# Kernel tuning notes

Measured on AMD Instinct MI355X. Metric: run time of the kernel, lower is better.

The kernel has to match this reference:

```python
import jax, jax.numpy as jnp
import numpy as np

N_NODES = 100000
N_EDGES = 6400000
N_ORDERS = 4
EPO = N_EDGES // N_ORDERS  # edges per order
K = 10


def setup_inputs() -> dict:
    key = jax.random.key(0)
    ks = jax.random.split(key, 7)
    x = jax.random.normal(ks[0], (N_NODES, K), dtype=jnp.float32)
    w_mp = jax.random.normal(ks[1], (K, 2 * K), dtype=jnp.float32) * (1.0 / np.sqrt(2 * K))
    b_mp = jax.random.normal(ks[2], (K,), dtype=jnp.float32) * 0.01
    w_out = jax.random.normal(ks[3], (K, K), dtype=jnp.float32) * (1.0 / np.sqrt(K))
    b_out = jax.random.normal(ks[4], (K,), dtype=jnp.float32) * 0.01
    edge_index = jax.random.randint(ks[5], (2, N_EDGES), 0, N_NODES, dtype=jnp.int64)
    orders = jax.random.randint(ks[6], (N_ORDERS, EPO), 0, N_EDGES, dtype=jnp.int64)
    return {"x": x, "w_mp": w_mp, "b_mp": b_mp, "w_out": w_out,
            "b_out": b_out, "edge_index": edge_index, "orders": orders}


def reference(x, w_mp, b_mp, w_out, b_out, edge_index, orders):
    n = x.shape[0]

    def step(h, order_idx):
        ei = edge_index[:, order_idx]            # [2, EPO] edges of this order
        # torch code swaps rows [1,0] before propagate, so in PyG terms:
        # source j = original row 1, target i = original row 0
        dst = ei[0]
        src = ei[1]
        x_i = h[dst]                             # [EPO, K]
        x_j = h[src]                             # [EPO, K]
        msg_in = jnp.concatenate([x_i, x_j - x_i], axis=1)   # [EPO, 2K]
        msg = msg_in @ w_mp.T + b_mp             # [EPO, K]
        aggr = jax.ops.segment_sum(msg, dst, num_segments=n)  # scatter-add
        return aggr + h, None                    # update(): aggr_out + x

    h, _ = jax.lax.scan(step, x, orders)
    return h @ w_out.T + b_out
```

## Files before the change

### kernel.cpp

```cpp
#include <hip/hip_runtime.h>

#define BLK 256
#define CAPB 4608
#define MAXNBD 512
#define MAXK2 2048
#define OVFN 65536
#define WBITS 13
#define W1CAP 8928
#define MAXNW 1024
#define IPTA 32
#define IPT2 18

__global__ void k_init_h(const float* __restrict__ x, float* __restrict__ h, int n) {
    int total = n * 16;
    int gs = gridDim.x * blockDim.x;
    for (int i = blockIdx.x * blockDim.x + threadIdx.x; i < total; i += gs) {
        int row = i >> 4, col = i & 15;
        h[i] = (col < 10) ? x[row * 10 + col] : 0.0f;
    }
}

__global__ __launch_bounds__(512) void k_win(const int* __restrict__ orders,
                                             int total, int epo, int NW,
                                             int* __restrict__ gcnt1,
                                             unsigned* __restrict__ recs1,
                                             int* __restrict__ ovf1_cnt,
                                             unsigned* __restrict__ ovf1) {
    __shared__ int bcnt[MAXNW];
    __shared__ int gbase[MAXNW];
    int t = threadIdx.x;
    for (int i = t; i < NW; i += 512) bcnt[i] = 0;
    __syncthreads();

    size_t base = (size_t)blockIdx.x * (512 * IPTA);
    int st0 = (int)(base / (size_t)epo);
    size_t b1 = (size_t)(st0 + 1) * (size_t)epo;

    unsigned recr[IPTA]; int rr[IPTA];
    #pragma unroll
    for (int q = 0; q < IPTA; ++q) {
        size_t g = base + (size_t)q * 512 + t;
        recr[q] = 0xFFFFFFFFu; rr[q] = 0;
        if (g < (size_t)total) {
            int idx = orders[g];
            int st = (g >= b1) ? (st0 + 1) : st0;
            recr[q] = ((unsigned)st << 23) | (unsigned)idx;
            rr[q] = atomicAdd(&bcnt[idx >> WBITS], 1);
        }
    }
    __syncthreads();
    for (int k = t; k < NW; k += 512) {
        int c = bcnt[k];
        gbase[k] = c ? atomicAdd(&gcnt1[k], c) : 0;
    }
    __syncthreads();
    #pragma unroll
    for (int q = 0; q < IPTA; ++q) {
        if (recr[q] != 0xFFFFFFFFu) {
            int idx = (int)(recr[q] & 0x7FFFFFu);
            int key = idx >> WBITS;
            int pos = gbase[key] + rr[q];
            if (pos < W1CAP)
                recs1[(size_t)key * W1CAP + pos] = recr[q];
            else {
                int o = atomicAdd(ovf1_cnt, 1);
                if (o < OVFN) ovf1[o] = recr[q];
            }
        }
    }
}

__global__ __launch_bounds__(512) void k_bin2(const int* __restrict__ ei, int ne,
                                              const int* __restrict__ gcnt1,
                                              const unsigned* __restrict__ recs1,
                                              int NW, int NBD,
                                              int* __restrict__ gcnt2,
                                              unsigned* __restrict__ recs2,
                                              int* __restrict__ ovf2_cnt,
                                              int2* __restrict__ ovf2) {
    __shared__ int cnt2[MAXK2];
    __shared__ int gbase[MAXK2];
    int t = threadIdx.x;
    int K2 = 4 * NBD;
    for (int i = t; i < K2; i += 512) cnt2[i] = 0;
    __syncthreads();

    int w = blockIdx.x;
    int c = gcnt1[w]; if (c > W1CAP) c = W1CAP;
    const unsigned* strm = recs1 + (size_t)w * W1CAP;

    unsigned recr[IPT2];
    #pragma unroll
    for (int q = 0; q < IPT2; ++q) {
        int r = q * 512 + t;
        recr[q] = (r < c) ? strm[r] : 0xFFFFFFFFu;
    }
    int dv[IPT2], sv[IPT2];
    #pragma unroll
    for (int q = 0; q < IPT2; ++q) {
        dv[q] = 0; sv[q] = 0;
        if (recr[q] != 0xFFFFFFFFu) {
            int idx = (int)(recr[q] & 0x7FFFFFu);
            dv[q] = ei[idx];
            sv[q] = ei[(size_t)ne + idx];
        }
    }
    int meta[IPT2];
    #pragma unroll
    for (int q = 0; q < IPT2; ++q) {
        meta[q] = -1;
        if (recr[q] != 0xFFFFFFFFu) {
            int st = (int)(recr[q] >> 23);
            int key = st * NBD + (dv[q] >> 8);
            int rk = atomicAdd(&cnt2[key], 1);
            meta[q] = (key << 14) | rk;
        }
    }
    __syncthreads();
    for (int k = t; k < K2; k += 512) {
        int cc = cnt2[k];
        gbase[k] = cc ? atomicAdd(&gcnt2[k], cc) : 0;
    }
    __syncthreads();
    #pragma unroll
    for (int q = 0; q < IPT2; ++q) {
        if (meta[q] >= 0) {
            int key = meta[q] >> 14, rk = meta[q] & 16383;
            int pos = gbase[key] + rk;
            unsigned r2 = ((unsigned)(dv[q] & 255) << 20) | (unsigned)sv[q];
            if (pos < CAPB)
                recs2[(size_t)key * CAPB + pos] = r2;
            else {
                int o = atomicAdd(ovf2_cnt, 1);
                if (o < OVFN) {
                    int st = (int)(recr[q] >> 23);
                    ovf2[o] = make_int2((st << 18) | dv[q], sv[q]);
                }
            }
        }
    }
}

#define IPTG ((CAPB + 511) / 512)
template<bool FINAL>
__global__ __launch_bounds__(512) void k_agg2(const float* __restrict__ h_cur,
                                              float* __restrict__ h_next,
                                              const int* __restrict__ gcnt2_st,
                                              const unsigned* __restrict__ recs2_st,
                                              const float* __restrict__ w_mp,
                                              const float* __restrict__ b_mp,
                                              const float* __restrict__ w_out,
                                              const float* __restrict__ b_out,
                                              float* __restrict__ out, int n) {
    __shared__ unsigned srt[CAPB];
    __shared__ int cnts[256];
    __shared__ int sc[256];
    __shared__ int offs[257];
    __shared__ float part[256 * 10];
    __shared__ float Wa[100], Wb[100], Bm[10];
    __shared__ float Wo[100], Bo[10];
    int t = threadIdx.x;
    if (t < 100) {
        int k = t / 10, j = t - k * 10;
        float w1 = w_mp[k * 20 + j];
        float w2 = w_mp[k * 20 + 10 + j];
        Wa[t] = w1 - w2; Wb[t] = w2;
        if (FINAL) Wo[t] = w_out[t];
    }
    if (t < 10) { Bm[t] = b_mp[t]; if (FINAL) Bo[t] = b_out[t]; }
    if (t < 256) cnts[t] = 0;
    __syncthreads();

    int bkt = blockIdx.x;
    int cnt = gcnt2_st[bkt];
    if (cnt > CAPB) cnt = CAPB;
    const unsigned* strm = recs2_st + (size_t)bkt * CAPB;

    unsigned myrec[IPTG];
    #pragma unroll
    for (int q = 0; q < IPTG; ++q) {
        int r = q * 512 + t;
        myrec[q] = 0xFFFFFFFFu;
        if (r < cnt) {
            unsigned rec = strm[r];
            myrec[q] = rec;
            atomicAdd(&cnts[rec >> 20], 1);
        }
    }
    __syncthreads();

    if (t < 256) sc[t] = cnts[t];
    __syncthreads();
    for (int off = 1; off < 256; off <<= 1) {
        int v = (t < 256 && t >= off) ? sc[t - off] : 0;
        __syncthreads();
        if (t < 256) sc[t] += v;
        __syncthreads();
    }
    if (t < 256) offs[t + 1] = sc[t];
    if (t == 0) offs[0] = 0;
    __syncthreads();
    if (t < 256) cnts[t] = offs[t];
    __syncthreads();

    #pragma unroll
    for (int q = 0; q < IPTG; ++q) {
        if (myrec[q] != 0xFFFFFFFFu) {
            int pos = atomicAdd(&cnts[myrec[q] >> 20], 1);
            srt[pos] = myrec[q];
        }
    }
    __syncthreads();

    int node = t & 255, half = t >> 8;
    int b0 = offs[node], m = offs[node + 1] - b0;
    float S[10] = {0,0,0,0,0,0,0,0,0,0};
    for (int p = b0 + half; p < b0 + m; p += 2) {
        int s = (int)(srt[p] & 0xFFFFFu);
        const float* pj = h_cur + (size_t)s * 16;
        float4 a0 = *(const float4*)(pj);
        float4 a1 = *(const float4*)(pj + 4);
        float2 a2 = *(const float2*)(pj + 8);
        S[0] += a0.x; S[1] += a0.y; S[2] += a0.z; S[3] += a0.w;
        S[4] += a1.x; S[5] += a1.y; S[6] += a1.z; S[7] += a1.w;
        S[8] += a2.x; S[9] += a2.y;
    }
    if (half == 1) {
        #pragma unroll
        for (int j = 0; j < 10; ++j) part[node * 10 + j] = S[j];
    }
    __syncthreads();
    if (half == 0) {
        int i = bkt * 256 + node;
        if (i < n) {
            #pragma unroll
            for (int j = 0; j < 10; ++j) S[j] += part[node * 10 + j];
            const float* pi = h_cur + (size_t)i * 16;
            float4 x0 = *(const float4*)(pi);
            float4 x1 = *(const float4*)(pi + 4);
            float2 x2 = *(const float2*)(pi + 8);
            float xi[10] = {x0.x, x0.y, x0.z, x0.w, x1.x, x1.y, x1.z, x1.w, x2.x, x2.y};
            float deg = (float)m;
            float o[10];
            #pragma unroll
            for (int k = 0; k < 10; ++k) {
                float ma = Bm[k];
                float mb = 0.0f;
                #pragma unroll
                for (int j = 0; j < 10; ++j) {
                    ma += Wa[k * 10 + j] * xi[j];
                    mb += Wb[k * 10 + j] * S[j];
                }
                o[k] = xi[k] + deg * ma + mb;
            }
            if (FINAL) {
                float q2[10];
                #pragma unroll
                for (int k = 0; k < 10; ++k) {
                    float m2 = Bo[k];
                    #pragma unroll
                    for (int j = 0; j < 10; ++j) m2 += Wo[k * 10 + j] * o[j];
                    q2[k] = m2;
                }
                float* po = out + (size_t)i * 10;
                *(float2*)(po)     = make_float2(q2[0], q2[1]);
                *(float2*)(po + 2) = make_float2(q2[2], q2[3]);
                *(float2*)(po + 4) = make_float2(q2[4], q2[5]);
                *(float2*)(po + 6) = make_float2(q2[6], q2[7]);
                *(float2*)(po + 8) = make_float2(q2[8], q2[9]);
            } else {
                float* po = h_next + (size_t)i * 16;
                *(float4*)(po)     = make_float4(o[0], o[1], o[2], o[3]);
                *(float4*)(po + 4) = make_float4(o[4], o[5], o[6], o[7]);
                *(float2*)(po + 8) = make_float2(o[8], o[9]);
            }
        }
    }
}

__global__ void k_fix(const float* __restrict__ h_cur, float* __restrict__ h_next,
                      const int* __restrict__ ei, int ne,
                      const int* __restrict__ ovf1_cnt, const unsigned* __restrict__ ovf1,
                      const int* __restrict__ ovf2_cnt, const int2* __restrict__ ovf2,
                      const float* __restrict__ w_mp, const float* __restrict__ b_mp,
                      int st) {
    __shared__ float Wa[100], Wb[100], Bm[10];
    int t = threadIdx.x;
    if (t < 100) {
        int k = t / 10, j = t - k * 10;
        float w1 = w_mp[k * 20 + j];
        float w2 = w_mp[k * 20 + 10 + j];
        Wa[t] = w1 - w2; Wb[t] = w2;
    }
    if (t < 10) Bm[t] = b_mp[t];
    __syncthreads();
    int c1 = *ovf1_cnt; if (c1 > OVFN) c1 = OVFN;
    int c2 = *ovf2_cnt; if (c2 > OVFN) c2 = OVFN;
    int gs = gridDim.x * blockDim.x;
    for (int i = blockIdx.x * blockDim.x + t; i < c1 + c2; i += gs) {
        int d, s;
        if (i < c1) {
            unsigned v = ovf1[i];
            if ((int)(v >> 23) != st) continue;
            int idx = (int)(v & 0x7FFFFFu);
            d = ei[idx]; s = ei[(size_t)ne + idx];
        } else {
            int2 p = ovf2[i - c1];
            if ((p.x >> 18) != st) continue;
            d = p.x & 0x3FFFF; s = p.y;
        }
        const float* pi = h_cur + (size_t)d * 16;
        const float* pj = h_cur + (size_t)s * 16;
        float xi[10], xj[10];
        #pragma unroll
        for (int j = 0; j < 10; ++j) { xi[j] = pi[j]; xj[j] = pj[j]; }
        float* po = h_next + (size_t)d * 16;
        #pragma unroll
        for (int k = 0; k < 10; ++k) {
            float m = Bm[k];
            #pragma unroll
            for (int j = 0; j < 10; ++j) m += Wa[k * 10 + j] * xi[j] + Wb[k * 10 + j] * xj[j];
            atomicAdd(po + k, m);
        }
    }
}

__global__ void k_fix_final(const float* __restrict__ h_cur, float* __restrict__ out,
                            const int* __restrict__ ei, int ne,
                            const int* __restrict__ ovf1_cnt, const unsigned* __restrict__ ovf1,
                            const int* __restrict__ ovf2_cnt, const int2* __restrict__ ovf2,
                            const float* __restrict__ w_mp, const float* __restrict__ b_mp,
                            const float* __restrict__ w_out, int st) {
    __shared__ float Wa[100], Wb[100], Bm[10], Wo[100];
    int t = threadIdx.x;
    if (t < 100) {
        int k = t / 10, j = t - k * 10;
        float w1 = w_mp[k * 20 + j];
        float w2 = w_mp[k * 20 + 10 + j];
        Wa[t] = w1 - w2; Wb[t] = w2;
        Wo[t] = w_out[t];
    }
    if (t < 10) Bm[t] = b_mp[t];
    __syncthreads();
    int c1 = *ovf1_cnt; if (c1 > OVFN) c1 = OVFN;
    int c2 = *ovf2_cnt; if (c2 > OVFN) c2 = OVFN;
    int gs = gridDim.x * blockDim.x;
    for (int i = blockIdx.x * blockDim.x + t; i < c1 + c2; i += gs) {
        int d, s;
        if (i < c1) {
            unsigned v = ovf1[i];
            if ((int)(v >> 23) != st) continue;
            int idx = (int)(v & 0x7FFFFFu);
            d = ei[idx]; s = ei[(size_t)ne + idx];
        } else {
            int2 p = ovf2[i - c1];
            if ((p.x >> 18) != st) continue;
            d = p.x & 0x3FFFF; s = p.y;
        }
        const float* pi = h_cur + (size_t)d * 16;
        const float* pj = h_cur + (size_t)s * 16;
        float xi[10], xj[10];
        #pragma unroll
        for (int j = 0; j < 10; ++j) { xi[j] = pi[j]; xj[j] = pj[j]; }
        float dm[10];
        #pragma unroll
        for (int k = 0; k < 10; ++k) {
            float m = Bm[k];
            #pragma unroll
            for (int j = 0; j < 10; ++j) m += Wa[k * 10 + j] * xi[j] + Wb[k * 10 + j] * xj[j];
            dm[k] = m;
        }
        float* po = out + (size_t)d * 10;
        #pragma unroll
        for (int q = 0; q < 10; ++q) {
            float m = 0.0f;
            #pragma unroll
            for (int k = 0; k < 10; ++k) m += Wo[q * 10 + k] * dm[k];
            atomicAdd(po + q, m);
        }
    }
}


__global__ void k_init10(const float* __restrict__ x, float* __restrict__ h, int n10) {
    int gs = gridDim.x * blockDim.x;
    for (int i = blockIdx.x * blockDim.x + threadIdx.x; i < n10; i += gs) h[i] = x[i];
}
__global__ void k_copy4(const float4* __restrict__ src, float4* __restrict__ dst, int n4) {
    int gs = gridDim.x * blockDim.x;
    for (int i = blockIdx.x * blockDim.x + threadIdx.x; i < n4; i += gs) dst[i] = src[i];
}
__global__ void k_edge_step10(const float* __restrict__ h_cur, float* __restrict__ h_next,
                              const int* __restrict__ edge_index, const int* __restrict__ order,
                              const float* __restrict__ w_mp, const float* __restrict__ b_mp,
                              int epo, int ne) {
    __shared__ float Wc[200]; __shared__ float Bc[10];
    int t = threadIdx.x;
    if (t < 200) {
        int k = t / 20, j = t - k * 20;
        float w = w_mp[t];
        Wc[t] = (j < 10) ? (w - w_mp[k * 20 + j + 10]) : w;
    }
    if (t < 10) Bc[t] = b_mp[t];
    __syncthreads();
    int gs = gridDim.x * blockDim.x;
    for (int e = blockIdx.x * blockDim.x + t; e < epo; e += gs) {
        int idx = order[e];
        int dst = edge_index[idx];
        int src = edge_index[(size_t)ne + idx];
        const float* pi = h_cur + (size_t)dst * 10;
        const float* pj = h_cur + (size_t)src * 10;
        float xi[10], xj[10];
        #pragma unroll
        for (int j = 0; j < 10; ++j) { xi[j] = pi[j]; xj[j] = pj[j]; }
        float* po = h_next + (size_t)dst * 10;
        #pragma unroll
        for (int k = 0; k < 10; ++k) {
            float m = Bc[k];
            #pragma unroll
            for (int j = 0; j < 10; ++j) m += Wc[k * 20 + j] * xi[j] + Wc[k * 20 + 10 + j] * xj[j];
            atomicAdd(po + k, m);
        }
    }
}
__global__ void k_out10(const float* __restrict__ h, const float* __restrict__ w_out,
                        const float* __restrict__ b_out, float* __restrict__ out, int n) {
    __shared__ float W[100]; __shared__ float B[10];
    int t = threadIdx.x;
    if (t < 100) W[t] = w_out[t];
    if (t < 10)  B[t] = b_out[t];
    __syncthreads();
    int gs = gridDim.x * blockDim.x;
    for (int i = blockIdx.x * blockDim.x + t; i < n; i += gs) {
        float xi[10];
        #pragma unroll
        for (int j = 0; j < 10; ++j) xi[j] = h[(size_t)i * 10 + j];
        #pragma unroll
        for (int k = 0; k < 10; ++k) {
            float m = B[k];
            #pragma unroll
            for (int j = 0; j < 10; ++j) m += W[k * 10 + j] * xi[j];
            out[(size_t)i * 10 + k] = m;
        }
    }
}


extern "C" void kernel_launch(void* const* d_in, const int* in_sizes, int n_in,
                              void* d_out, int out_size, void* d_ws, size_t ws_size,
                              hipStream_t stream) {
    const float* x      = (const float*)d_in[0];
    const float* w_mp   = (const float*)d_in[1];
    const float* b_mp   = (const float*)d_in[2];
    const float* w_out  = (const float*)d_in[3];
    const float* b_out  = (const float*)d_in[4];
    const int*   edge_i = (const int*)d_in[5];
    const int*   orders = (const int*)d_in[6];

    int n  = in_sizes[0] / 10;
    int ne = in_sizes[5] / 2;
    const int n_orders = 4;
    int epo = in_sizes[6] / n_orders;
    int total = n_orders * epo;

    float* out = (float*)d_out;

    int NBD = (n + 255) >> 8;
    int NW  = (ne + (1 << WBITS) - 1) >> WBITS;

    size_t off_hA    = 0;
    size_t off_hB    = off_hA + (size_t)n * 16;
    size_t off_recs1 = off_hB + (size_t)n * 16;
    size_t off_recs2 = off_recs1 + (size_t)NW * W1CAP;
    size_t off_ovf2  = off_recs2 + (size_t)4 * NBD * CAPB;
    size_t off_ovf1  = off_ovf2 + (size_t)2 * OVFN;
    size_t off_gcnt1 = off_ovf1 + OVFN;
    size_t off_gcnt2 = off_gcnt1 + NW;
    size_t off_cnts  = off_gcnt2 + (size_t)4 * NBD;
    size_t need      = (off_cnts + 2) * 4;

    bool ok = (ws_size >= need) && (NW <= MAXNW) && (NBD <= MAXNBD) &&
              (4 * NBD <= MAXK2) && (ne <= (1 << 23)) && (n < (1 << 17));

    if (!ok) {
        float* hA = (float*)d_ws;
        float* hB = hA + (size_t)n * 10;
        int n10 = n * 10;
        hipLaunchKernelGGL(k_init10, dim3(min((n10 + BLK - 1) / BLK, 2048)), dim3(BLK), 0, stream,
                           x, hA, n10);
        int n4 = n10 / 4;
        float* cur = hA; float* nxt = hB;
        int gb_edge = min((epo + BLK - 1) / BLK, 6400);
        for (int s = 0; s < n_orders; ++s) {
            hipLaunchKernelGGL(k_copy4, dim3(min((n4 + BLK - 1) / BLK, 2048)), dim3(BLK), 0, stream,
                               (const float4*)cur, (float4*)nxt, n4);
            hipLaunchKernelGGL(k_edge_step10, dim3(gb_edge), dim3(BLK), 0, stream,
                               cur, nxt, edge_i, orders + (size_t)s * epo, w_mp, b_mp, epo, ne);
            float* t2 = cur; cur = nxt; nxt = t2;
        }
        hipLaunchKernelGGL(k_out10, dim3(min((n + BLK - 1) / BLK, 2048)), dim3(BLK), 0, stream,
                           cur, w_out, b_out, out, n);
        return;
    }

    float*    hA      = (float*)d_ws;
    float*    hB      = (float*)d_ws + off_hB;
    unsigned* recs1   = (unsigned*)d_ws + off_recs1;
    unsigned* recs2   = (unsigned*)d_ws + off_recs2;
    int2*     ovf2    = (int2*)((int*)d_ws + off_ovf2);
    unsigned* ovf1    = (unsigned*)d_ws + off_ovf1;
    int*      gcnt1   = (int*)d_ws + off_gcnt1;
    int*      gcnt2   = (int*)d_ws + off_gcnt2;
    int*      ovfcnts = (int*)d_ws + off_cnts;

    hipMemsetAsync(gcnt1, 0, ((size_t)NW + (size_t)4 * NBD + 2) * sizeof(int), stream);

    int gb_init = min((n * 16 + BLK - 1) / BLK, 2048);
    hipLaunchKernelGGL(k_init_h, dim3(gb_init), dim3(BLK), 0, stream, x, hA, n);

    int gbA = (total + 512 * IPTA - 1) / (512 * IPTA);
    hipLaunchKernelGGL(k_win, dim3(gbA), dim3(512), 0, stream,
                       orders, total, epo, NW, gcnt1, recs1, ovfcnts + 0, ovf1);

    hipLaunchKernelGGL(k_bin2, dim3(NW), dim3(512), 0, stream,
                       edge_i, ne, gcnt1, recs1, NW, NBD,
                       gcnt2, recs2, ovfcnts + 1, ovf2);

    float* cur = hA; float* nxt = hB;
    for (int s = 0; s < n_orders; ++s) {
        bool fin = (s == n_orders - 1);
        if (fin) {
            hipLaunchKernelGGL((k_agg2<true>), dim3(NBD), dim3(512), 0, stream,
                               cur, nxt, gcnt2 + (size_t)s * NBD,
                               recs2 + (size_t)s * NBD * CAPB, w_mp, b_mp,
                               w_out, b_out, out, n);
            hipLaunchKernelGGL(k_fix_final, dim3(8), dim3(256), 0, stream,
                               cur, out, edge_i, ne,
                               ovfcnts + 0, ovf1, ovfcnts + 1, ovf2,
                               w_mp, b_mp, w_out, s);
        } else {
            hipLaunchKernelGGL((k_agg2<false>), dim3(NBD), dim3(512), 0, stream,
                               cur, nxt, gcnt2 + (size_t)s * NBD,
                               recs2 + (size_t)s * NBD * CAPB, w_mp, b_mp,
                               w_out, b_out, out, n);
            hipLaunchKernelGGL(k_fix, dim3(8), dim3(256), 0, stream,
                               cur, nxt, edge_i, ne,
                               ovfcnts + 0, ovf1, ovfcnts + 1, ovf2,
                               w_mp, b_mp, s);
            float* t2 = cur; cur = nxt; nxt = t2;
        }
    }
}
```

Baseline: 286.7 us.

## Partition edge binning per order to shrink shared counters and defer source loads

```diff
diff --git a/kernel.cpp b/kernel.cpp
--- a/kernel.cpp
+++ b/kernel.cpp
@@ -1,15 +1,14 @@
 #include <hip/hip_runtime.h>
 
 #define BLK 256
+#define WBITS 13
+#define W1CAPS 2432
 #define CAPB 4608
+#define MAXNW 1024
 #define MAXNBD 512
-#define MAXK2 2048
 #define OVFN 65536
-#define WBITS 13
-#define W1CAP 8928
-#define MAXNW 1024
-#define IPTA 32
-#define IPT2 18
+#define IPTA 16
+#define NSL 20
 
 __global__ void k_init_h(const float* __restrict__ x, float* __restrict__ h, int n) {
     int total = n * 16;
@@ -21,7 +20,7 @@
 }
 
 __global__ __launch_bounds__(512) void k_win(const int* __restrict__ orders,
-                                             int total, int epo, int NW,
+                                             int epo, int NW, int TPS,
                                              int* __restrict__ gcnt1,
                                              unsigned* __restrict__ recs1,
                                              int* __restrict__ ovf1_cnt,
@@ -29,42 +28,39 @@
     __shared__ int bcnt[MAXNW];
     __shared__ int gbase[MAXNW];
     int t = threadIdx.x;
+    int st = blockIdx.x / TPS;
+    int tb = blockIdx.x % TPS;
     for (int i = t; i < NW; i += 512) bcnt[i] = 0;
     __syncthreads();
 
-    size_t base = (size_t)blockIdx.x * (512 * IPTA);
-    int st0 = (int)(base / (size_t)epo);
-    size_t b1 = (size_t)(st0 + 1) * (size_t)epo;
-
-    unsigned recr[IPTA]; int rr[IPTA];
+    const int* ord = orders + (size_t)st * epo + (size_t)tb * (512 * IPTA);
+    int lim = epo - tb * (512 * IPTA);
+
+    int idxs[IPTA]; int rr[IPTA];
     #pragma unroll
     for (int q = 0; q < IPTA; ++q) {
-        size_t g = base + (size_t)q * 512 + t;
-        recr[q] = 0xFFFFFFFFu; rr[q] = 0;
-        if (g < (size_t)total) {
-            int idx = orders[g];
-            int st = (g >= b1) ? (st0 + 1) : st0;
-            recr[q] = ((unsigned)st << 23) | (unsigned)idx;
-            rr[q] = atomicAdd(&bcnt[idx >> WBITS], 1);
-        }
-    }
+        int e = q * 512 + t;
+        idxs[q] = (e < lim) ? ord[e] : -1;
+    }
+    #pragma unroll
+    for (int q = 0; q < IPTA; ++q)
+        rr[q] = (idxs[q] >= 0) ? atomicAdd(&bcnt[idxs[q] >> WBITS], 1) : 0;
     __syncthreads();
     for (int k = t; k < NW; k += 512) {
         int c = bcnt[k];
-        gbase[k] = c ? atomicAdd(&gcnt1[k], c) : 0;
+        gbase[k] = c ? atomicAdd(&gcnt1[st * NW + k], c) : 0;
     }
     __syncthreads();
     #pragma unroll
     for (int q = 0; q < IPTA; ++q) {
-        if (recr[q] != 0xFFFFFFFFu) {
-            int idx = (int)(recr[q] & 0x7FFFFFu);
-            int key = idx >> WBITS;
-            int pos = gbase[key] + rr[q];
-            if (pos < W1CAP)
-                recs1[(size_t)key * W1CAP + pos] = recr[q];
+        if (idxs[q] >= 0) {
+            int w = idxs[q] >> WBITS;
+            int pos = gbase[w] + rr[q];
+            if (pos < W1CAPS)
+                recs1[((size_t)st * NW + w) * W1CAPS + pos] = (unsigned)idxs[q];
             else {
                 int o = atomicAdd(ovf1_cnt, 1);
-                if (o < OVFN) ovf1[o] = recr[q];
+                if (o < OVFN) ovf1[o] = ((unsigned)st << 23) | (unsigned)idxs[q];
             }
         }
     }
@@ -73,69 +69,69 @@
 __global__ __launch_bounds__(512) void k_bin2(const int* __restrict__ ei, int ne,
                                               const int* __restrict__ gcnt1,
                                               const unsigned* __restrict__ recs1,
-                                              int NW, int NBD,
+                                              int NW, int NWG, int NBD,
                                               int* __restrict__ gcnt2,
                                               unsigned* __restrict__ recs2,
                                               int* __restrict__ ovf2_cnt,
                                               int2* __restrict__ ovf2) {
-    __shared__ int cnt2[MAXK2];
-    __shared__ int gbase[MAXK2];
-    int t = threadIdx.x;
-    int K2 = 4 * NBD;
-    for (int i = t; i < K2; i += 512) cnt2[i] = 0;
-    __syncthreads();
-
-    int w = blockIdx.x;
-    int c = gcnt1[w]; if (c > W1CAP) c = W1CAP;
-    const unsigned* strm = recs1 + (size_t)w * W1CAP;
-
-    unsigned recr[IPT2];
-    #pragma unroll
-    for (int q = 0; q < IPT2; ++q) {
-        int r = q * 512 + t;
-        recr[q] = (r < c) ? strm[r] : 0xFFFFFFFFu;
-    }
-    int dv[IPT2], sv[IPT2];
-    #pragma unroll
-    for (int q = 0; q < IPT2; ++q) {
-        dv[q] = 0; sv[q] = 0;
-        if (recr[q] != 0xFFFFFFFFu) {
-            int idx = (int)(recr[q] & 0x7FFFFFu);
-            dv[q] = ei[idx];
-            sv[q] = ei[(size_t)ne + idx];
-        }
-    }
-    int meta[IPT2];
-    #pragma unroll
-    for (int q = 0; q < IPT2; ++q) {
-        meta[q] = -1;
-        if (recr[q] != 0xFFFFFFFFu) {
-            int st = (int)(recr[q] >> 23);
-            int key = st * NBD + (dv[q] >> 8);
-            int rk = atomicAdd(&cnt2[key], 1);
-            meta[q] = (key << 14) | rk;
-        }
-    }
-    __syncthreads();
-    for (int k = t; k < K2; k += 512) {
-        int cc = cnt2[k];
-        gbase[k] = cc ? atomicAdd(&gcnt2[k], cc) : 0;
-    }
-    __syncthreads();
-    #pragma unroll
-    for (int q = 0; q < IPT2; ++q) {
-        if (meta[q] >= 0) {
-            int key = meta[q] >> 14, rk = meta[q] & 16383;
+    __shared__ int cnt2[MAXNBD];
+    __shared__ int gbase[MAXNBD];
+    int t = threadIdx.x;
+    int st = blockIdx.x / NWG;
+    int wg = blockIdx.x % NWG;
+    for (int i = t; i < NBD; i += 512) cnt2[i] = 0;
+    __syncthreads();
+
+    int segc[4];
+    #pragma unroll
+    for (int g = 0; g < 4; ++g) {
+        int w = wg * 4 + g;
+        int c = (w < NW) ? gcnt1[st * NW + w] : 0;
+        segc[g] = (c < W1CAPS) ? c : W1CAPS;
+    }
+
+    int idxs[NSL];
+    #pragma unroll
+    for (int g = 0; g < 4; ++g) {
+        const unsigned* strm = recs1 + ((size_t)st * NW + wg * 4 + g) * W1CAPS;
+        #pragma unroll
+        for (int q = 0; q < 5; ++q) {
+            int r = q * 512 + t;
+            idxs[g * 5 + q] = (r < segc[g]) ? (int)strm[r] : -1;
+        }
+    }
+    int dv[NSL];
+    #pragma unroll
+    for (int s2 = 0; s2 < NSL; ++s2)
+        dv[s2] = (idxs[s2] >= 0) ? ei[idxs[s2]] : 0;
+    int meta[NSL];
+    #pragma unroll
+    for (int s2 = 0; s2 < NSL; ++s2) {
+        meta[s2] = -1;
+        if (idxs[s2] >= 0) {
+            int rk = atomicAdd(&cnt2[dv[s2] >> 8], 1);
+            meta[s2] = (dv[s2] << 14) | rk;
+        }
+    }
+    __syncthreads();
+    for (int k = t; k < NBD; k += 512) {
+        int c = cnt2[k];
+        gbase[k] = c ? atomicAdd(&gcnt2[st * NBD + k], c) : 0;
+    }
+    __syncthreads();
+    #pragma unroll
+    for (int s2 = 0; s2 < NSL; ++s2) {
+        if (meta[s2] >= 0) {
+            int s = ei[(size_t)ne + idxs[s2]];
+            int d = meta[s2] >> 14, rk = meta[s2] & 16383;
+            int key = d >> 8;
             int pos = gbase[key] + rk;
-            unsigned r2 = ((unsigned)(dv[q] & 255) << 20) | (unsigned)sv[q];
+            unsigned r2 = ((unsigned)(d & 255) << 20) | (unsigned)s;
             if (pos < CAPB)
-                recs2[(size_t)key * CAPB + pos] = r2;
+                recs2[((size_t)st * NBD + key) * CAPB + pos] = r2;
             else {
                 int o = atomicAdd(ovf2_cnt, 1);
-                if (o < OVFN) {
-                    int st = (int)(recr[q] >> 23);
-                    ovf2[o] = make_int2((st << 18) | dv[q], sv[q]);
-                }
+                if (o < OVFN) ovf2[o] = make_int2((st << 18) | d, s);
             }
         }
     }
@@ -461,26 +457,27 @@
     int ne = in_sizes[5] / 2;
     const int n_orders = 4;
     int epo = in_sizes[6] / n_orders;
-    int total = n_orders * epo;
 
     float* out = (float*)d_out;
 
     int NBD = (n + 255) >> 8;
     int NW  = (ne + (1 << WBITS) - 1) >> WBITS;
+    int NWG = (NW + 3) / 4;
+    int TPS = (epo + 512 * IPTA - 1) / (512 * IPTA);
 
     size_t off_hA    = 0;
     size_t off_hB    = off_hA + (size_t)n * 16;
     size_t off_recs1 = off_hB + (size_t)n * 16;
-    size_t off_recs2 = off_recs1 + (size_t)NW * W1CAP;
+    size_t off_recs2 = off_recs1 + (size_t)4 * NW * W1CAPS;
     size_t off_ovf2  = off_recs2 + (size_t)4 * NBD * CAPB;
     size_t off_ovf1  = off_ovf2 + (size_t)2 * OVFN;
     size_t off_gcnt1 = off_ovf1 + OVFN;
-    size_t off_gcnt2 = off_gcnt1 + NW;
+    size_t off_gcnt2 = off_gcnt1 + (size_t)4 * NW;
     size_t off_cnts  = off_gcnt2 + (size_t)4 * NBD;
     size_t need      = (off_cnts + 2) * 4;
 
     bool ok = (ws_size >= need) && (NW <= MAXNW) && (NBD <= MAXNBD) &&
-              (4 * NBD <= MAXK2) && (ne <= (1 << 23)) && (n < (1 << 17));
+              (ne <= (1 << 23)) && (n < (1 << 17)) && (4 * W1CAPS < 16384);
 
     if (!ok) {
         float* hA = (float*)d_ws;
@@ -513,17 +510,16 @@
     int*      gcnt2   = (int*)d_ws + off_gcnt2;
     int*      ovfcnts = (int*)d_ws + off_cnts;
 
-    hipMemsetAsync(gcnt1, 0, ((size_t)NW + (size_t)4 * NBD + 2) * sizeof(int), stream);
+    hipMemsetAsync(gcnt1, 0, ((size_t)4 * NW + (size_t)4 * NBD + 2) * sizeof(int), stream);
 
     int gb_init = min((n * 16 + BLK - 1) / BLK, 2048);
     hipLaunchKernelGGL(k_init_h, dim3(gb_init), dim3(BLK), 0, stream, x, hA, n);
 
-    int gbA = (total + 512 * IPTA - 1) / (512 * IPTA);
-    hipLaunchKernelGGL(k_win, dim3(gbA), dim3(512), 0, stream,
-                       orders, total, epo, NW, gcnt1, recs1, ovfcnts + 0, ovf1);
-
-    hipLaunchKernelGGL(k_bin2, dim3(NW), dim3(512), 0, stream,
-                       edge_i, ne, gcnt1, recs1, NW, NBD,
+    hipLaunchKernelGGL(k_win, dim3(4 * TPS), dim3(512), 0, stream,
+                       orders, epo, NW, TPS, gcnt1, recs1, ovfcnts + 0, ovf1);
+
+    hipLaunchKernelGGL(k_bin2, dim3(4 * NWG), dim3(512), 0, stream,
+                       edge_i, ne, gcnt1, recs1, NW, NWG, NBD,
                        gcnt2, recs2, ovfcnts + 1, ovf2);
 
     float* cur = hA; float* nxt = hB;
```

Measured after the change: 325.1 us. +13.4%, slower.

## Pad second-level bucket runs to 16 and widen windows in edge binning

Applied to the files above, without the earlier changes.

```diff
diff --git a/kernel.cpp b/kernel.cpp
--- a/kernel.cpp
+++ b/kernel.cpp
@@ -1,15 +1,16 @@
 #include <hip/hip_runtime.h>
 
 #define BLK 256
-#define CAPB 4608
+#define WBITS 14
+#define W1CAP 17408
+#define CAPBP 7168
+#define MAXNW 512
+#define MAXK2 2048
 #define MAXNBD 512
-#define MAXK2 2048
 #define OVFN 65536
-#define WBITS 13
-#define W1CAP 8928
-#define MAXNW 1024
 #define IPTA 32
-#define IPT2 18
+#define NSL2 17
+#define SENT 0xFFFFFFFFu
 
 __global__ void k_init_h(const float* __restrict__ x, float* __restrict__ h, int n) {
     int total = n * 16;
@@ -40,7 +41,7 @@
     #pragma unroll
     for (int q = 0; q < IPTA; ++q) {
         size_t g = base + (size_t)q * 512 + t;
-        recr[q] = 0xFFFFFFFFu; rr[q] = 0;
+        recr[q] = SENT; rr[q] = 0;
         if (g < (size_t)total) {
             int idx = orders[g];
             int st = (g >= b1) ? (st0 + 1) : st0;
@@ -56,7 +57,7 @@
     __syncthreads();
     #pragma unroll
     for (int q = 0; q < IPTA; ++q) {
-        if (recr[q] != 0xFFFFFFFFu) {
+        if (recr[q] != SENT) {
             int idx = (int)(recr[q] & 0x7FFFFFu);
             int key = idx >> WBITS;
             int pos = gbase[key] + rr[q];
@@ -70,78 +71,84 @@
     }
 }
 
-__global__ __launch_bounds__(512) void k_bin2(const int* __restrict__ ei, int ne,
-                                              const int* __restrict__ gcnt1,
-                                              const unsigned* __restrict__ recs1,
-                                              int NW, int NBD,
-                                              int* __restrict__ gcnt2,
-                                              unsigned* __restrict__ recs2,
-                                              int* __restrict__ ovf2_cnt,
-                                              int2* __restrict__ ovf2) {
+__global__ __launch_bounds__(1024) void k_bin2(const int* __restrict__ ei, int ne,
+                                               const int* __restrict__ gcnt1,
+                                               const unsigned* __restrict__ recs1,
+                                               int NW, int NBD,
+                                               int* __restrict__ gcnt2,
+                                               unsigned* __restrict__ recs2,
+                                               int* __restrict__ ovf2_cnt,
+                                               int2* __restrict__ ovf2) {
     __shared__ int cnt2[MAXK2];
     __shared__ int gbase[MAXK2];
     int t = threadIdx.x;
     int K2 = 4 * NBD;
-    for (int i = t; i < K2; i += 512) cnt2[i] = 0;
+    for (int i = t; i < K2; i += 1024) cnt2[i] = 0;
     __syncthreads();
 
     int w = blockIdx.x;
     int c = gcnt1[w]; if (c > W1CAP) c = W1CAP;
     const unsigned* strm = recs1 + (size_t)w * W1CAP;
 
-    unsigned recr[IPT2];
-    #pragma unroll
-    for (int q = 0; q < IPT2; ++q) {
-        int r = q * 512 + t;
-        recr[q] = (r < c) ? strm[r] : 0xFFFFFFFFu;
-    }
-    int dv[IPT2], sv[IPT2];
-    #pragma unroll
-    for (int q = 0; q < IPT2; ++q) {
-        dv[q] = 0; sv[q] = 0;
-        if (recr[q] != 0xFFFFFFFFu) {
-            int idx = (int)(recr[q] & 0x7FFFFFu);
-            dv[q] = ei[idx];
-            sv[q] = ei[(size_t)ne + idx];
-        }
-    }
-    int meta[IPT2];
-    #pragma unroll
-    for (int q = 0; q < IPT2; ++q) {
-        meta[q] = -1;
-        if (recr[q] != 0xFFFFFFFFu) {
-            int st = (int)(recr[q] >> 23);
+    int recr[NSL2];
+    #pragma unroll
+    for (int q = 0; q < NSL2; ++q) {
+        int r = q * 1024 + t;
+        recr[q] = (r < c) ? (int)strm[r] : -1;
+    }
+    int dv[NSL2];
+    #pragma unroll
+    for (int q = 0; q < NSL2; ++q)
+        dv[q] = (recr[q] >= 0) ? ei[recr[q] & 0x7FFFFF] : 0;
+    unsigned meta[NSL2];
+    #pragma unroll
+    for (int q = 0; q < NSL2; ++q) {
+        meta[q] = SENT;
+        if (recr[q] >= 0) {
+            int st = (int)(((unsigned)recr[q]) >> 23);
             int key = st * NBD + (dv[q] >> 8);
             int rk = atomicAdd(&cnt2[key], 1);
-            meta[q] = (key << 14) | rk;
-        }
-    }
-    __syncthreads();
-    for (int k = t; k < K2; k += 512) {
+            meta[q] = ((unsigned)dv[q] << 15) | (unsigned)rk;
+        }
+    }
+    __syncthreads();
+    for (int k = t; k < K2; k += 1024) {
         int cc = cnt2[k];
-        gbase[k] = cc ? atomicAdd(&gcnt2[k], cc) : 0;
-    }
-    __syncthreads();
-    #pragma unroll
-    for (int q = 0; q < IPT2; ++q) {
-        if (meta[q] >= 0) {
-            int key = meta[q] >> 14, rk = meta[q] & 16383;
+        gbase[k] = cc ? atomicAdd(&gcnt2[k], (cc + 15) & ~15) : 0;
+    }
+    __syncthreads();
+    #pragma unroll
+    for (int q = 0; q < NSL2; ++q) {
+        if (meta[q] != SENT) {
+            int idx = recr[q] & 0x7FFFFF;
+            int st  = (int)(((unsigned)recr[q]) >> 23);
+            int s = ei[(size_t)ne + idx];
+            int d = (int)(meta[q] >> 15);
+            int rk = (int)(meta[q] & 0x7FFFu);
+            int key = st * NBD + (d >> 8);
             int pos = gbase[key] + rk;
-            unsigned r2 = ((unsigned)(dv[q] & 255) << 20) | (unsigned)sv[q];
-            if (pos < CAPB)
-                recs2[(size_t)key * CAPB + pos] = r2;
+            unsigned r2 = ((unsigned)(d & 255) << 20) | (unsigned)s;
+            if (pos < CAPBP)
+                recs2[(size_t)key * CAPBP + pos] = r2;
             else {
                 int o = atomicAdd(ovf2_cnt, 1);
-                if (o < OVFN) {
-                    int st = (int)(recr[q] >> 23);
-                    ovf2[o] = make_int2((st << 18) | dv[q], sv[q]);
-                }
+                if (o < OVFN) ovf2[o] = make_int2((st << 18) | d, s);
             }
         }
     }
-}
-
-#define IPTG ((CAPB + 511) / 512)
+    for (int k = t; k < K2; k += 1024) {
+        int cc = cnt2[k];
+        if (cc) {
+            int b0 = gbase[k];
+            int pe = b0 + ((cc + 15) & ~15);
+            if (pe > CAPBP) pe = CAPBP;
+            unsigned* sp = recs2 + (size_t)k * CAPBP;
+            for (int p = b0 + cc; p < pe; ++p) sp[p] = SENT;
+        }
+    }
+}
+
+#define IPTG ((CAPBP + 511) / 512)
 template<bool FINAL>
 __global__ __launch_bounds__(512) void k_agg2(const float* __restrict__ h_cur,
                                               float* __restrict__ h_next,
@@ -152,7 +159,7 @@
                                               const float* __restrict__ w_out,
                                               const float* __restrict__ b_out,
                                               float* __restrict__ out, int n) {
-    __shared__ unsigned srt[CAPB];
+    __shared__ unsigned srt[CAPBP];
     __shared__ int cnts[256];
     __shared__ int sc[256];
     __shared__ int offs[257];
@@ -173,18 +180,20 @@
 
     int bkt = blockIdx.x;
     int cnt = gcnt2_st[bkt];
-    if (cnt > CAPB) cnt = CAPB;
-    const unsigned* strm = recs2_st + (size_t)bkt * CAPB;
+    if (cnt > CAPBP) cnt = CAPBP;
+    const unsigned* strm = recs2_st + (size_t)bkt * CAPBP;
 
     unsigned myrec[IPTG];
     #pragma unroll
     for (int q = 0; q < IPTG; ++q) {
         int r = q * 512 + t;
-        myrec[q] = 0xFFFFFFFFu;
+        myrec[q] = SENT;
         if (r < cnt) {
             unsigned rec = strm[r];
-            myrec[q] = rec;
-            atomicAdd(&cnts[rec >> 20], 1);
+            if (rec != SENT) {
+                myrec[q] = rec;
+                atomicAdd(&cnts[rec >> 20], 1);
+            }
         }
     }
     __syncthreads();
@@ -205,7 +214,7 @@
 
     #pragma unroll
     for (int q = 0; q < IPTG; ++q) {
-        if (myrec[q] != 0xFFFFFFFFu) {
+        if (myrec[q] != SENT) {
             int pos = atomicAdd(&cnts[myrec[q] >> 20], 1);
             srt[pos] = myrec[q];
         }
@@ -467,20 +476,21 @@
 
     int NBD = (n + 255) >> 8;
     int NW  = (ne + (1 << WBITS) - 1) >> WBITS;
+    int K2  = 4 * NBD;
 
     size_t off_hA    = 0;
     size_t off_hB    = off_hA + (size_t)n * 16;
     size_t off_recs1 = off_hB + (size_t)n * 16;
     size_t off_recs2 = off_recs1 + (size_t)NW * W1CAP;
-    size_t off_ovf2  = off_recs2 + (size_t)4 * NBD * CAPB;
+    size_t off_ovf2  = off_recs2 + (size_t)K2 * CAPBP;
     size_t off_ovf1  = off_ovf2 + (size_t)2 * OVFN;
     size_t off_gcnt1 = off_ovf1 + OVFN;
     size_t off_gcnt2 = off_gcnt1 + NW;
-    size_t off_cnts  = off_gcnt2 + (size_t)4 * NBD;
+    size_t off_cnts  = off_gcnt2 + K2;
     size_t need      = (off_cnts + 2) * 4;
 
     bool ok = (ws_size >= need) && (NW <= MAXNW) && (NBD <= MAXNBD) &&
-              (4 * NBD <= MAXK2) && (ne <= (1 << 23)) && (n < (1 << 17));
+              (K2 <= MAXK2) && (ne <= (1 << 23)) && (n < (1 << 17));
 
     if (!ok) {
         float* hA = (float*)d_ws;
@@ -513,7 +523,7 @@
     int*      gcnt2   = (int*)d_ws + off_gcnt2;
     int*      ovfcnts = (int*)d_ws + off_cnts;
 
-    hipMemsetAsync(gcnt1, 0, ((size_t)NW + (size_t)4 * NBD + 2) * sizeof(int), stream);
+    hipMemsetAsync(gcnt1, 0, ((size_t)NW + (size_t)K2 + 2) * sizeof(int), stream);
 
     int gb_init = min((n * 16 + BLK - 1) / BLK, 2048);
     hipLaunchKernelGGL(k_init_h, dim3(gb_init), dim3(BLK), 0, stream, x, hA, n);
@@ -522,7 +532,7 @@
     hipLaunchKernelGGL(k_win, dim3(gbA), dim3(512), 0, stream,
                        orders, total, epo, NW, gcnt1, recs1, ovfcnts + 0, ovf1);
 
-    hipLaunchKernelGGL(k_bin2, dim3(NW), dim3(512), 0, stream,
+    hipLaunchKernelGGL(k_bin2, dim3(NW), dim3(1024), 0, stream,
                        edge_i, ne, gcnt1, recs1, NW, NBD,
                        gcnt2, recs2, ovfcnts + 1, ovf2);
 
@@ -532,7 +542,7 @@
         if (fin) {
             hipLaunchKernelGGL((k_agg2<true>), dim3(NBD), dim3(512), 0, stream,
                                cur, nxt, gcnt2 + (size_t)s * NBD,
-                               recs2 + (size_t)s * NBD * CAPB, w_mp, b_mp,
+                               recs2 + (size_t)s * NBD * CAPBP, w_mp, b_mp,
                                w_out, b_out, out, n);
             hipLaunchKernelGGL(k_fix_final, dim3(8), dim3(256), 0, stream,
                                cur, out, edge_i, ne,
@@ -541,7 +551,7 @@
         } else {
             hipLaunchKernelGGL((k_agg2<false>), dim3(NBD), dim3(512), 0, stream,
                                cur, nxt, gcnt2 + (size_t)s * NBD,
-                               recs2 + (size_t)s * NBD * CAPB, w_mp, b_mp,
+                               recs2 + (size_t)s * NBD * CAPBP, w_mp, b_mp,
                                w_out, b_out, out, n);
             hipLaunchKernelGGL(k_fix, dim3(8), dim3(256), 0, stream,
                                cur, nxt, edge_i, ne,
```

Result: slower. 317.4 us (+10.7%).
